# Performance work log

Measured on AMD Instinct MI355X. Metric: run time of the kernel, lower is better.

The kernel has to match this reference:

```python
import jax, jax.numpy as jnp
import numpy as np

TEMP = 1.0
EPS = 1e-15

B, N, F, K = 8, 2000, 128, 64


def setup_inputs() -> dict:
    key = jax.random.key(0)
    k1, k2, k3 = jax.random.split(key, 3)
    x = jax.random.normal(k1, (B, N, F), dtype=jnp.float32)
    adj = jax.random.uniform(k2, (B, N, N), dtype=jnp.float32)
    s = jax.random.normal(k3, (B, N, K), dtype=jnp.float32)
    mask = jnp.ones((B, N), dtype=bool)
    return {"x": x, "adj": adj, "s": s, "mask": mask}


def reference(x, adj, s, mask):
    k = s.shape[-1]
    s = jax.nn.softmax(s / TEMP, axis=-1)
    m = mask[..., None].astype(x.dtype)          # [B,N,1]
    x = x * m
    s = s * m

    # pooled features: s^T x -> [B,K,F]
    out = jnp.einsum('bnk,bnf->bkf', s, x)

    # pooled adjacency: s^T A s -> [B,K,K]
    as_ = jnp.einsum('bnm,bmk->bnk', adj, s)     # A s, [B,N,K]
    out_adj = jnp.einsum('bnk,bnl->bkl', as_, s)

    # mincut loss
    mincut_num = jnp.einsum('bkk->b', out_adj)
    d_flat = jnp.sum(adj, axis=-1)               # degree, [B,N]
    # trace(s^T diag(d) s) = sum_n d_n * sum_k s_nk^2 (avoids dense diag)
    mincut_den = jnp.einsum('bn,bnk,bnk->b', d_flat, s, s)
    mincut_loss = jnp.mean(-(mincut_num / mincut_den))

    # orthogonality loss
    ss = jnp.einsum('bnk,bnl->bkl', s, s)        # [B,K,K]
    ss_norm = jnp.linalg.norm(ss, axis=(-2, -1), keepdims=True)
    i_s = jnp.eye(k, dtype=ss.dtype)
    ortho = jnp.linalg.norm(ss / ss_norm - i_s / jnp.sqrt(jnp.asarray(k, ss.dtype)), axis=(-2, -1))
    ortho_loss = jnp.mean(ortho)

    # zero diagonal, symmetric degree normalization
    ind = jnp.arange(k)
    out_adj = out_adj.at[:, ind, ind].set(0.0)
    d = jnp.sqrt(jnp.sum(out_adj, axis=-1))[:, None, :] + EPS  # [B,1,K]
    out_adj = out_adj / d / jnp.swapaxes(d, 1, 2)

    return out, out_adj, mincut_loss, ortho_loss
```

## Files before the change

### kernel.cpp

```cpp
#include <hip/hip_runtime.h>

typedef __bf16 bf16;
typedef __bf16 bf16x4 __attribute__((ext_vector_type(4)));
typedef __bf16 bf16x8 __attribute__((ext_vector_type(8)));
typedef float f32x4 __attribute__((ext_vector_type(4)));

#define NB 8
#define NN 2000
#define N2 2048
#define KK 64
#define FF 128

__global__ __launch_bounds__(256) void k1_softmax(const float* __restrict__ s,
                                                  bf16* __restrict__ sT,
                                                  float* __restrict__ rowsq) {
  const int b = blockIdx.x >> 5, tile = blockIdx.x & 31;
  const int n0 = tile * 64;
  const int t = threadIdx.x;
  const int r = t >> 2, q = t & 3;
  __shared__ float ptile[64][65];
  const int n = n0 + r;
  const bool valid = n < NN;
  float v[16];
  if (valid) {
    const float4* src = (const float4*)(s + ((size_t)(b * NN + n)) * KK + q * 16);
#pragma unroll
    for (int i = 0; i < 4; ++i) {
      float4 f = src[i];
      v[4 * i + 0] = f.x; v[4 * i + 1] = f.y; v[4 * i + 2] = f.z; v[4 * i + 3] = f.w;
    }
  } else {
#pragma unroll
    for (int i = 0; i < 16; ++i) v[i] = 0.f;
  }
  float mx = v[0];
#pragma unroll
  for (int i = 1; i < 16; ++i) mx = fmaxf(mx, v[i]);
  mx = fmaxf(mx, __shfl_xor(mx, 1));
  mx = fmaxf(mx, __shfl_xor(mx, 2));
  float sum = 0.f;
#pragma unroll
  for (int i = 0; i < 16; ++i) { v[i] = __expf(v[i] - mx); sum += v[i]; }
  sum += __shfl_xor(sum, 1);
  sum += __shfl_xor(sum, 2);
  const float scale = valid ? (1.0f / sum) : 0.f;
  float rq = 0.f;
#pragma unroll
  for (int i = 0; i < 16; ++i) { v[i] *= scale; rq += v[i] * v[i]; }
  rq += __shfl_xor(rq, 1);
  rq += __shfl_xor(rq, 2);
  if (q == 0) rowsq[b * N2 + n0 + r] = rq;
#pragma unroll
  for (int i = 0; i < 16; ++i) ptile[r][q * 16 + i] = v[i];
  __syncthreads();
  bf16x8 o0, o1;
#pragma unroll
  for (int i = 0; i < 8; ++i) o0[i] = (bf16)ptile[q * 16 + i][r];
#pragma unroll
  for (int i = 0; i < 8; ++i) o1[i] = (bf16)ptile[q * 16 + 8 + i][r];
  bf16* dst = sT + ((size_t)(b * KK + r)) * N2 + n0 + q * 16;
  *(bf16x8*)dst = o0;
  *(bf16x8*)(dst + 8) = o1;
}

__global__ __launch_bounds__(1024, 8) void k2_big(const float* __restrict__ adj,
                                                  const bf16* __restrict__ sT,
                                                  const float* __restrict__ x,
                                                  bf16* __restrict__ xT,
                                                  bf16* __restrict__ asT,
                                                  const float* __restrict__ rowsq,
                                                  float* __restrict__ den_part) {
  __shared__ __align__(16) char smem[69632];
  __shared__ float dredS[16];
  const int bid0 = blockIdx.x;
  const int t = threadIdx.x;

  if (bid0 >= 256) {
    const int lg2 = ((bid0 - 256) & 7) * 32 + ((bid0 - 256) >> 3);
    const int bb = lg2 >> 5, tl = lg2 & 31;
    const int n0b = tl * 64;
    float* xt = (float*)smem;
#pragma unroll
    for (int i = 0; i < 2; ++i) {
      int idx = t + 1024 * i;
      int row = idx >> 5, c4 = idx & 31;
      int n = n0b + row;
      float4 vv = make_float4(0.f, 0.f, 0.f, 0.f);
      if (n < NN) vv = ((const float4*)(x + ((size_t)(bb * NN + n)) * FF))[c4];
      *(float4*)&xt[row * 132 + c4 * 4] = vv;
    }
    __syncthreads();
    const int f = t >> 3, h = t & 7;
    bf16x8 o;
#pragma unroll
    for (int i = 0; i < 8; ++i) o[i] = (bf16)xt[(h * 8 + i) * 132 + f];
    *(bf16x8*)(xT + ((size_t)(bb * FF + f)) * N2 + n0b + h * 8) = o;
    return;
  }

  const int lgc = (bid0 & 7) * 32 + (bid0 >> 3);
  const int b = lgc >> 5, tile = lgc & 31;
  const int n0 = tile * 64;

  const int w = t >> 6, l = t & 63;
  const int lr = l & 15, lg = l >> 4;
  const int nr = w & 3, kr = w >> 2;

  const int srow = t >> 4, scp = t & 15;
  const bool avalid = (n0 + srow) < NN;
  const float4* arowp = (const float4*)(adj +
      ((size_t)(b * NN) + (avalid ? (n0 + srow) : 0)) * NN);
  const bf16* sTrp = sT + ((size_t)(b * KK + srow)) * N2;

  const int afo = (nr * 16 + lr) * 136;
  const int bfo = 8704 + (kr * 16 + lr) * 136;

  f32x4 acc;
#pragma unroll
  for (int r = 0; r < 4; ++r) acc[r] = 0.f;

  float4 a0A, a1A, a0B, a1B;
  bf16x8 bA, bB;

#define K2_LOAD(C, LA0, LA1, LB)                                            \
  {                                                                         \
    const int base_ = (C) * 32 + scp * 2;                                   \
    const int i0_ = base_ > 499 ? 499 : base_;                              \
    const int i1_ = base_ + 1 > 499 ? 499 : base_ + 1;                      \
    if (avalid) { LA0 = arowp[i0_]; LA1 = arowp[i1_]; }                     \
    else { LA0 = make_float4(0.f,0.f,0.f,0.f); LA1 = LA0; }                 \
    LB = *(const bf16x8*)(sTrp + (C) * 128 + scp * 8);                      \
  }

#define K2_WRITE(BUF, LA0, LA1, LB)                                         \
  {                                                                         \
    bf16x8 av_;                                                             \
    av_[0] = (bf16)LA0.x; av_[1] = (bf16)LA0.y;                             \
    av_[2] = (bf16)LA0.z; av_[3] = (bf16)LA0.w;                             \
    av_[4] = (bf16)LA1.x; av_[5] = (bf16)LA1.y;                             \
    av_[6] = (bf16)LA1.z; av_[7] = (bf16)LA1.w;                             \
    bf16* p_ = (bf16*)smem + (BUF) * 17408 + srow * 136 + scp * 8;          \
    *(bf16x8*)p_ = av_;                                                     \
    *(bf16x8*)(p_ + 8704) = LB;                                             \
  }

#define K2_MFMA(BUF)                                                        \
  {                                                                         \
    const bf16* base_ = (bf16*)smem + (BUF) * 17408;                        \
    _Pragma("unroll")                                                       \
    for (int ms = 0; ms < 4; ++ms) {                                        \
      bf16x8 af_ = *(const bf16x8*)(base_ + afo + ms * 32 + lg * 8);        \
      bf16x8 bf_ = *(const bf16x8*)(base_ + bfo + ms * 32 + lg * 8);        \
      acc = __builtin_amdgcn_mfma_f32_16x16x32_bf16(af_, bf_, acc, 0, 0, 0);\
    }                                                                       \
  }

  K2_LOAD(0, a0A, a1A, bA);
  K2_WRITE(0, a0A, a1A, bA);
  K2_LOAD(1, a0B, a1B, bB);
  __syncthreads();
  for (int cc = 0; cc < 7; ++cc) {
    const int c = cc * 2;
    K2_LOAD(c + 2, a0A, a1A, bA);
    K2_MFMA(0);
    K2_WRITE(1, a0B, a1B, bB);
    __syncthreads();
    K2_LOAD(c + 3, a0B, a1B, bB);
    K2_MFMA(1);
    K2_WRITE(0, a0A, a1A, bA);
    __syncthreads();
  }
  K2_MFMA(0);
  K2_WRITE(1, a0B, a1B, bB);
  __syncthreads();
  K2_MFMA(1);
#undef K2_LOAD
#undef K2_WRITE
#undef K2_MFMA

  bf16x4 o;
#pragma unroll
  for (int r = 0; r < 4; ++r) o[r] = (bf16)acc[r];
  *(bf16x4*)(asT + ((size_t)(b * KK + kr * 16 + lr)) * N2 + n0 + nr * 16 + lg * 4) = o;

  float s0 = acc[0], s1 = acc[1], s2 = acc[2], s3 = acc[3];
#pragma unroll
  for (int off = 1; off <= 8; off <<= 1) {
    s0 += __shfl_xor(s0, off); s1 += __shfl_xor(s1, off);
    s2 += __shfl_xor(s2, off); s3 += __shfl_xor(s3, off);
  }
  const float* rqp = rowsq + b * N2 + n0 + nr * 16 + lg * 4;
  float part = s0 * rqp[0] + s1 * rqp[1] + s2 * rqp[2] + s3 * rqp[3];
  part += __shfl_xor(part, 16);
  part += __shfl_xor(part, 32);
  if (l == 0) dredS[w] = part;
  __syncthreads();
  if (t == 0) {
    float dt = 0.f;
#pragma unroll
    for (int i = 0; i < 16; ++i) dt += dredS[i];
    den_part[b * 32 + tile] = dt;
  }
}

__global__ __launch_bounds__(256) void k3_gemms(const bf16* __restrict__ sT,
                                                const bf16* __restrict__ asT,
                                                const bf16* __restrict__ xT,
                                                float* __restrict__ adjraw,
                                                float* __restrict__ ssw,
                                                float* __restrict__ dout) {
  const int lgc = (blockIdx.x & 7) * 64 + (blockIdx.x >> 3);
  const int b = lgc >> 6, u = lgc & 63;
  const bf16 *Ab, *Bb;
  float* Cb;
  int ldC;
  if (u < 16) {
    const int rt = u >> 2, ct = u & 3;
    Ab = asT + ((size_t)(b * KK + rt * 16)) * N2;
    Bb = sT + ((size_t)(b * KK + ct * 16)) * N2;
    Cb = adjraw + b * KK * KK + rt * 16 * KK + ct * 16; ldC = KK;
  } else if (u < 32) {
    const int v = u - 16, rt = v >> 2, ct = v & 3;
    Ab = sT + ((size_t)(b * KK + rt * 16)) * N2;
    Bb = sT + ((size_t)(b * KK + ct * 16)) * N2;
    Cb = ssw + b * KK * KK + rt * 16 * KK + ct * 16; ldC = KK;
  } else {
    const int v = u - 32, rt = v >> 3, ct = v & 7;
    Ab = sT + ((size_t)(b * KK + rt * 16)) * N2;
    Bb = xT + ((size_t)(b * FF + ct * 16)) * N2;
    Cb = dout + b * KK * FF + rt * 16 * FF + ct * 16; ldC = FF;
  }
  const int t = threadIdx.x;
  const int w = t >> 6, l = t & 63;
  const int lr = l & 15, lg = l >> 4;
  f32x4 acc;
#pragma unroll
  for (int r = 0; r < 4; ++r) acc[r] = 0.f;
  const int m_begin = w * 512;
#pragma unroll 4
  for (int s = 0; s < 16; ++s) {
    const int m = m_begin + s * 32 + lg * 8;
    bf16x8 af = *(const bf16x8*)(Ab + (size_t)lr * N2 + m);
    bf16x8 bfv = *(const bf16x8*)(Bb + (size_t)lr * N2 + m);
    acc = __builtin_amdgcn_mfma_f32_16x16x32_bf16(af, bfv, acc, 0, 0, 0);
  }
  __shared__ float red[4][16][16];
#pragma unroll
  for (int r = 0; r < 4; ++r) red[w][lg * 4 + r][lr] = acc[r];
  __syncthreads();
  const int row = t >> 4, col = t & 15;
  const float v = red[0][row][col] + red[1][row][col] +
                  red[2][row][col] + red[3][row][col];
  Cb[row * ldC + col] = v;
}

__device__ inline float wred64(float v) {
#pragma unroll
  for (int off = 32; off > 0; off >>= 1) v += __shfl_xor(v, off);
  return v;
}

__global__ __launch_bounds__(512) void k4_final(const float* __restrict__ adjraw,
                                                const float* __restrict__ ssw,
                                                const float* __restrict__ den_part,
                                                float* __restrict__ dout) {
  const int b = threadIdx.x >> 6;
  const int lane = threadIdx.x & 63;
  const float dp = (lane < 32) ? den_part[b * 32 + lane] : 0.f;
  const float den = wred64(dp);
  const float* arow = adjraw + b * 4096 + lane * 64;
  float4 av[16];
#pragma unroll
  for (int i = 0; i < 16; ++i) av[i] = ((const float4*)arow)[i];
  const float diag = adjraw[b * 4096 + lane * 65];
  float rs = 0.f;
#pragma unroll
  for (int i = 0; i < 16; ++i) rs += av[i].x + av[i].y + av[i].z + av[i].w;
  rs -= diag;
  rs = fmaxf(rs, 0.f);
  const float num = wred64(diag);
  const float d = sqrtf(rs) + 1e-15f;
  __shared__ float dsh[8][64];
  __shared__ float lossm[8], losso[8];
  dsh[b][lane] = d;
  __syncthreads();
  const float invd = 1.0f / d;
  float* orow = dout + NB * KK * FF + b * 4096 + lane * 64;
#pragma unroll
  for (int i = 0; i < 16; ++i) {
    float4 cvv = av[i];
    cvv.x = (4 * i + 0 == lane) ? 0.f : cvv.x * invd / dsh[b][4 * i + 0];
    cvv.y = (4 * i + 1 == lane) ? 0.f : cvv.y * invd / dsh[b][4 * i + 1];
    cvv.z = (4 * i + 2 == lane) ? 0.f : cvv.z * invd / dsh[b][4 * i + 2];
    cvv.w = (4 * i + 3 == lane) ? 0.f : cvv.w * invd / dsh[b][4 * i + 3];
    ((float4*)orow)[i] = cvv;
  }
  const float* srow = ssw + b * 4096 + lane * 64;
  float4 sv[16];
  float sq = 0.f;
#pragma unroll
  for (int i = 0; i < 16; ++i) {
    sv[i] = ((const float4*)srow)[i];
    sq += sv[i].x * sv[i].x + sv[i].y * sv[i].y + sv[i].z * sv[i].z + sv[i].w * sv[i].w;
  }
  const float frob = sqrtf(wred64(sq));
  const float fi = 1.0f / frob;
  float osum = 0.f;
#pragma unroll
  for (int i = 0; i < 16; ++i) {
    float tx = sv[i].x * fi - ((4 * i + 0 == lane) ? 0.125f : 0.f);
    float ty = sv[i].y * fi - ((4 * i + 1 == lane) ? 0.125f : 0.f);
    float tz = sv[i].z * fi - ((4 * i + 2 == lane) ? 0.125f : 0.f);
    float tw = sv[i].w * fi - ((4 * i + 3 == lane) ? 0.125f : 0.f);
    osum += tx * tx + ty * ty + tz * tz + tw * tw;
  }
  const float ot = wred64(osum);
  if (lane == 0) {
    lossm[b] = -(num / den);
    losso[b] = sqrtf(ot);
  }
  __syncthreads();
  if (threadIdx.x == 0) {
    float m = 0.f, oo = 0.f;
#pragma unroll
    for (int b2 = 0; b2 < 8; ++b2) { m += lossm[b2]; oo += losso[b2]; }
    dout[NB * KK * FF + NB * KK * KK + 0] = m * 0.125f;
    dout[NB * KK * FF + NB * KK * KK + 1] = oo * 0.125f;
  }
}

extern "C" void kernel_launch(void* const* d_in, const int* in_sizes, int n_in,
                              void* d_out, int out_size, void* d_ws, size_t ws_size,
                              hipStream_t stream) {
  const float* x = (const float*)d_in[0];
  const float* adj = (const float*)d_in[1];
  const float* s = (const float*)d_in[2];
  float* out = (float*)d_out;
  char* ws = (char*)d_ws;
  bf16* sT = (bf16*)ws;
  bf16* xT = (bf16*)(ws + (2u << 20));
  bf16* asT = (bf16*)(ws + (6u << 20));
  float* rowsq = (float*)(ws + (8u << 20));
  float* den_part = (float*)(ws + (8u << 20) + 65536);
  float* adjraw = (float*)(ws + (8u << 20) + 65536 + 4096);
  float* ssw = adjraw + NB * KK * KK;

  k1_softmax<<<256, 256, 0, stream>>>(s, sT, rowsq);
  k2_big<<<512, 1024, 0, stream>>>(adj, sT, x, xT, asT, rowsq, den_part);
  k3_gemms<<<512, 256, 0, stream>>>(sT, asT, xT, adjraw, ssw, out);
  k4_final<<<1, 512, 0, stream>>>(adjraw, ssw, den_part, out);
}
```

Measured before the change: 228.4 us.

## Split A·s GEMM into 32-row tiles with 512-thread blocks for more parallelism

The adjacency-times-assignment GEMM kernel now processes 32 rows of adj per block instead of 64, using 512 threads and 512 GEMM blocks (plus 256 x-transpose blocks) instead of 256+256. The sT operand tile is loaded redundantly per block, and the denominator partial sums go to 64 slots per batch instead of 32. The double-buffered pipeline becomes a single loop with fewer unrolled stages. The aim is to spread the memory-bound adj stream over more CUs and improve occupancy, at the cost of re-reading s twice as often and a smaller per-block reuse.

```diff
diff --git a/kernel.cpp b/kernel.cpp
--- a/kernel.cpp
+++ b/kernel.cpp
@@ -63,26 +63,26 @@
   *(bf16x8*)(dst + 8) = o1;
 }
 
-__global__ __launch_bounds__(1024, 8) void k2_big(const float* __restrict__ adj,
-                                                  const bf16* __restrict__ sT,
-                                                  const float* __restrict__ x,
-                                                  bf16* __restrict__ xT,
-                                                  bf16* __restrict__ asT,
-                                                  const float* __restrict__ rowsq,
-                                                  float* __restrict__ den_part) {
-  __shared__ __align__(16) char smem[69632];
-  __shared__ float dredS[16];
+__global__ __launch_bounds__(512, 6) void k2_big(const float* __restrict__ adj,
+                                                 const bf16* __restrict__ sT,
+                                                 const float* __restrict__ x,
+                                                 bf16* __restrict__ xT,
+                                                 bf16* __restrict__ asT,
+                                                 const float* __restrict__ rowsq,
+                                                 float* __restrict__ den_part) {
+  __shared__ __align__(16) char smem[52224];
+  __shared__ float dredS[8];
   const int bid0 = blockIdx.x;
   const int t = threadIdx.x;
 
-  if (bid0 >= 256) {
-    const int lg2 = ((bid0 - 256) & 7) * 32 + ((bid0 - 256) >> 3);
-    const int bb = lg2 >> 5, tl = lg2 & 31;
+  if (bid0 >= 512) {
+    const int q = bid0 - 512;
+    const int bb = q & 7, tl = q >> 3;
     const int n0b = tl * 64;
     float* xt = (float*)smem;
 #pragma unroll
-    for (int i = 0; i < 2; ++i) {
-      int idx = t + 1024 * i;
+    for (int i = 0; i < 4; ++i) {
+      int idx = t + 512 * i;
       int row = idx >> 5, c4 = idx & 31;
       int n = n0b + row;
       float4 vv = make_float4(0.f, 0.f, 0.f, 0.f);
@@ -90,63 +90,69 @@
       *(float4*)&xt[row * 132 + c4 * 4] = vv;
     }
     __syncthreads();
-    const int f = t >> 3, h = t & 7;
-    bf16x8 o;
-#pragma unroll
-    for (int i = 0; i < 8; ++i) o[i] = (bf16)xt[(h * 8 + i) * 132 + f];
-    *(bf16x8*)(xT + ((size_t)(bb * FF + f)) * N2 + n0b + h * 8) = o;
+    const int f = t >> 2, h = t & 3;
+    bf16x8 o0, o1;
+#pragma unroll
+    for (int i = 0; i < 8; ++i) o0[i] = (bf16)xt[(h * 16 + i) * 132 + f];
+#pragma unroll
+    for (int i = 0; i < 8; ++i) o1[i] = (bf16)xt[(h * 16 + 8 + i) * 132 + f];
+    bf16* dst = xT + ((size_t)(bb * FF + f)) * N2 + n0b + h * 16;
+    *(bf16x8*)dst = o0;
+    *(bf16x8*)(dst + 8) = o1;
     return;
   }
 
-  const int lgc = (bid0 & 7) * 32 + (bid0 >> 3);
-  const int b = lgc >> 5, tile = lgc & 31;
-  const int n0 = tile * 64;
+  const int b = bid0 & 7, tile = bid0 >> 3;
+  const int n0 = tile * 32;
 
   const int w = t >> 6, l = t & 63;
   const int lr = l & 15, lg = l >> 4;
-  const int nr = w & 3, kr = w >> 2;
+  const int nr = w & 1, kr = w >> 1;
 
   const int srow = t >> 4, scp = t & 15;
+  const int brow = t >> 3, bcol = t & 7;
   const bool avalid = (n0 + srow) < NN;
   const float4* arowp = (const float4*)(adj +
       ((size_t)(b * NN) + (avalid ? (n0 + srow) : 0)) * NN);
-  const bf16* sTrp = sT + ((size_t)(b * KK + srow)) * N2;
+  const bf16* sTrp = sT + ((size_t)(b * KK + brow)) * N2;
 
   const int afo = (nr * 16 + lr) * 136;
-  const int bfo = 8704 + (kr * 16 + lr) * 136;
+  const int bfo = 4352 + (kr * 16 + lr) * 136;
 
   f32x4 acc;
 #pragma unroll
   for (int r = 0; r < 4; ++r) acc[r] = 0.f;
 
-  float4 a0A, a1A, a0B, a1B;
-  bf16x8 bA, bB;
-
-#define K2_LOAD(C, LA0, LA1, LB)                                            \
+  float4 La0, La1;
+  bf16x8 Lb0, Lb1;
+
+#define K2_LOAD(C)                                                          \
   {                                                                         \
     const int base_ = (C) * 32 + scp * 2;                                   \
     const int i0_ = base_ > 499 ? 499 : base_;                              \
     const int i1_ = base_ + 1 > 499 ? 499 : base_ + 1;                      \
-    if (avalid) { LA0 = arowp[i0_]; LA1 = arowp[i1_]; }                     \
-    else { LA0 = make_float4(0.f,0.f,0.f,0.f); LA1 = LA0; }                 \
-    LB = *(const bf16x8*)(sTrp + (C) * 128 + scp * 8);                      \
-  }
-
-#define K2_WRITE(BUF, LA0, LA1, LB)                                         \
-  {                                                                         \
-    bf16x8 av_;                                                             \
-    av_[0] = (bf16)LA0.x; av_[1] = (bf16)LA0.y;                             \
-    av_[2] = (bf16)LA0.z; av_[3] = (bf16)LA0.w;                             \
-    av_[4] = (bf16)LA1.x; av_[5] = (bf16)LA1.y;                             \
-    av_[6] = (bf16)LA1.z; av_[7] = (bf16)LA1.w;                             \
-    bf16* p_ = (bf16*)smem + (BUF) * 17408 + srow * 136 + scp * 8;          \
-    *(bf16x8*)p_ = av_;                                                     \
-    *(bf16x8*)(p_ + 8704) = LB;                                             \
+    if (avalid) { La0 = arowp[i0_]; La1 = arowp[i1_]; }                     \
+    else { La0 = make_float4(0.f,0.f,0.f,0.f); La1 = La0; }                 \
+    Lb0 = *(const bf16x8*)(sTrp + (C) * 128 + bcol * 8);                    \
+    Lb1 = *(const bf16x8*)(sTrp + (C) * 128 + 64 + bcol * 8);               \
+  }
+
+#define K2_WRITE(BUF)                                                      \
+  {                                                                        \
+    bf16x8 av_;                                                            \
+    av_[0] = (bf16)La0.x; av_[1] = (bf16)La0.y;                            \
+    av_[2] = (bf16)La0.z; av_[3] = (bf16)La0.w;                            \
+    av_[4] = (bf16)La1.x; av_[5] = (bf16)La1.y;                            \
+    av_[6] = (bf16)La1.z; av_[7] = (bf16)La1.w;                            \
+    bf16* bb_ = (bf16*)smem + (BUF) * 13056;                               \
+    *(bf16x8*)(bb_ + srow * 136 + scp * 8) = av_;                          \
+    *(bf16x8*)(bb_ + 4352 + brow * 136 + bcol * 8) = Lb0;                  \
+    *(bf16x8*)(bb_ + 4352 + brow * 136 + 64 + bcol * 8) = Lb1;             \
   }
 
 #define K2_MFMA(BUF)                                                        \
   {                                                                         \
-    const bf16* base_ = (bf16*)smem + (BUF) * 17408;                        \
+    const bf16* base_ = (bf16*)smem + (BUF) * 13056;                        \
     _Pragma("unroll")                                                       \
     for (int ms = 0; ms < 4; ++ms) {                                        \
       bf16x8 af_ = *(const bf16x8*)(base_ + afo + ms * 32 + lg * 8);        \
@@ -155,25 +161,15 @@
     }                                                                       \
   }
 
-  K2_LOAD(0, a0A, a1A, bA);
-  K2_WRITE(0, a0A, a1A, bA);
-  K2_LOAD(1, a0B, a1B, bB);
-  __syncthreads();
-  for (int cc = 0; cc < 7; ++cc) {
-    const int c = cc * 2;
-    K2_LOAD(c + 2, a0A, a1A, bA);
-    K2_MFMA(0);
-    K2_WRITE(1, a0B, a1B, bB);
+  K2_LOAD(0);
+  K2_WRITE(0);
+  __syncthreads();
+  for (int c = 0; c < 16; ++c) {
+    if (c < 15) K2_LOAD(c + 1);
+    K2_MFMA(c & 1);
+    if (c < 15) K2_WRITE((c + 1) & 1);
     __syncthreads();
-    K2_LOAD(c + 3, a0B, a1B, bB);
-    K2_MFMA(1);
-    K2_WRITE(0, a0A, a1A, bA);
-    __syncthreads();
-  }
-  K2_MFMA(0);
-  K2_WRITE(1, a0B, a1B, bB);
-  __syncthreads();
-  K2_MFMA(1);
+  }
 #undef K2_LOAD
 #undef K2_WRITE
 #undef K2_MFMA
@@ -198,8 +194,8 @@
   if (t == 0) {
     float dt = 0.f;
 #pragma unroll
-    for (int i = 0; i < 16; ++i) dt += dredS[i];
-    den_part[b * 32 + tile] = dt;
+    for (int i = 0; i < 8; ++i) dt += dredS[i];
+    den_part[b * 64 + tile] = dt;
   }
 }
 
@@ -266,8 +262,7 @@
                                                 float* __restrict__ dout) {
   const int b = threadIdx.x >> 6;
   const int lane = threadIdx.x & 63;
-  const float dp = (lane < 32) ? den_part[b * 32 + lane] : 0.f;
-  const float den = wred64(dp);
+  const float den = wred64(den_part[b * 64 + lane]);
   const float* arow = adjraw + b * 4096 + lane * 64;
   float4 av[16];
 #pragma unroll
@@ -346,7 +341,7 @@
   float* ssw = adjraw + NB * KK * KK;
 
   k1_softmax<<<256, 256, 0, stream>>>(s, sT, rowsq);
-  k2_big<<<512, 1024, 0, stream>>>(adj, sT, x, xT, asT, rowsq, den_part);
+  k2_big<<<768, 512, 0, stream>>>(adj, sT, x, xT, asT, rowsq, den_part);
   k3_gemms<<<512, 256, 0, stream>>>(sT, asT, xT, adjraw, ssw, out);
   k4_final<<<1, 512, 0, stream>>>(adjraw, ssw, den_part, out);
 }
```

After: 230.5 us. Within noise of the previous version (+0.9%).

## Split adjacency GEMM along reduction dim into two halves for more blocks

Applied to the files above, without the earlier changes.

The A·s GEMM in k2 is split along the m (reduction) dimension into two halves, doubling the number of GEMM blocks from 256 to 512 so more CUs are busy streaming adj. Each half writes fp32 partial results to a new asP buffer, and k3 sums the two partials before converting to bf16 for the s^T(As) product. Degree-denominator partials are also split, and k4 reduces 64 entries instead of 32. This trades extra fp32 partial writes and reads, plus a larger workspace, for better occupancy on the memory-bound adj stream.

```diff
diff --git a/kernel.cpp b/kernel.cpp
--- a/kernel.cpp
+++ b/kernel.cpp
@@ -67,7 +67,7 @@
                                                   const bf16* __restrict__ sT,
                                                   const float* __restrict__ x,
                                                   bf16* __restrict__ xT,
-                                                  bf16* __restrict__ asT,
+                                                  float* __restrict__ asP,
                                                   const float* __restrict__ rowsq,
                                                   float* __restrict__ den_part) {
   __shared__ __align__(16) char smem[69632];
@@ -75,8 +75,9 @@
   const int bid0 = blockIdx.x;
   const int t = threadIdx.x;
 
-  if (bid0 >= 256) {
-    const int lg2 = ((bid0 - 256) & 7) * 32 + ((bid0 - 256) >> 3);
+  if (bid0 >= 512) {
+    const int q = bid0 - 512;
+    const int lg2 = (q & 7) * 32 + (q >> 3);
     const int bb = lg2 >> 5, tl = lg2 & 31;
     const int n0b = tl * 64;
     float* xt = (float*)smem;
@@ -98,9 +99,12 @@
     return;
   }
 
-  const int lgc = (bid0 & 7) * 32 + (bid0 >> 3);
-  const int b = lgc >> 5, tile = lgc & 31;
+  const int b = bid0 & 7;
+  const int idx = bid0 >> 3;
+  const int tile = idx & 31, half = idx >> 5;
   const int n0 = tile * 64;
+  const int mb4 = half * 256;
+  const int mbE = half * 1024;
 
   const int w = t >> 6, l = t & 63;
   const int lr = l & 15, lg = l >> 4;
@@ -119,29 +123,29 @@
 #pragma unroll
   for (int r = 0; r < 4; ++r) acc[r] = 0.f;
 
-  float4 a0A, a1A, a0B, a1B;
-  bf16x8 bA, bB;
-
-#define K2_LOAD(C, LA0, LA1, LB)                                            \
+  float4 La0, La1;
+  bf16x8 Lb;
+
+#define K2_LOAD(C)                                                          \
   {                                                                         \
-    const int base_ = (C) * 32 + scp * 2;                                   \
+    const int base_ = mb4 + (C) * 32 + scp * 2;                             \
     const int i0_ = base_ > 499 ? 499 : base_;                              \
     const int i1_ = base_ + 1 > 499 ? 499 : base_ + 1;                      \
-    if (avalid) { LA0 = arowp[i0_]; LA1 = arowp[i1_]; }                     \
-    else { LA0 = make_float4(0.f,0.f,0.f,0.f); LA1 = LA0; }                 \
-    LB = *(const bf16x8*)(sTrp + (C) * 128 + scp * 8);                      \
-  }
-
-#define K2_WRITE(BUF, LA0, LA1, LB)                                         \
+    if (avalid) { La0 = arowp[i0_]; La1 = arowp[i1_]; }                     \
+    else { La0 = make_float4(0.f,0.f,0.f,0.f); La1 = La0; }                 \
+    Lb = *(const bf16x8*)(sTrp + mbE + (C) * 128 + scp * 8);                \
+  }
+
+#define K2_WRITE(BUF)                                                       \
   {                                                                         \
     bf16x8 av_;                                                             \
-    av_[0] = (bf16)LA0.x; av_[1] = (bf16)LA0.y;                             \
-    av_[2] = (bf16)LA0.z; av_[3] = (bf16)LA0.w;                             \
-    av_[4] = (bf16)LA1.x; av_[5] = (bf16)LA1.y;                             \
-    av_[6] = (bf16)LA1.z; av_[7] = (bf16)LA1.w;                             \
+    av_[0] = (bf16)La0.x; av_[1] = (bf16)La0.y;                             \
+    av_[2] = (bf16)La0.z; av_[3] = (bf16)La0.w;                             \
+    av_[4] = (bf16)La1.x; av_[5] = (bf16)La1.y;                             \
+    av_[6] = (bf16)La1.z; av_[7] = (bf16)La1.w;                             \
     bf16* p_ = (bf16*)smem + (BUF) * 17408 + srow * 136 + scp * 8;          \
     *(bf16x8*)p_ = av_;                                                     \
-    *(bf16x8*)(p_ + 8704) = LB;                                             \
+    *(bf16x8*)(p_ + 8704) = Lb;                                             \
   }
 
 #define K2_MFMA(BUF)                                                        \
@@ -155,33 +159,21 @@
     }                                                                       \
   }
 
-  K2_LOAD(0, a0A, a1A, bA);
-  K2_WRITE(0, a0A, a1A, bA);
-  K2_LOAD(1, a0B, a1B, bB);
-  __syncthreads();
-  for (int cc = 0; cc < 7; ++cc) {
-    const int c = cc * 2;
-    K2_LOAD(c + 2, a0A, a1A, bA);
-    K2_MFMA(0);
-    K2_WRITE(1, a0B, a1B, bB);
+  K2_LOAD(0);
+  K2_WRITE(0);
+  __syncthreads();
+  for (int c = 0; c < 8; ++c) {
+    if (c < 7) K2_LOAD(c + 1);
+    K2_MFMA(c & 1);
+    if (c < 7) K2_WRITE((c + 1) & 1);
     __syncthreads();
-    K2_LOAD(c + 3, a0B, a1B, bB);
-    K2_MFMA(1);
-    K2_WRITE(0, a0A, a1A, bA);
-    __syncthreads();
-  }
-  K2_MFMA(0);
-  K2_WRITE(1, a0B, a1B, bB);
-  __syncthreads();
-  K2_MFMA(1);
+  }
 #undef K2_LOAD
 #undef K2_WRITE
 #undef K2_MFMA
 
-  bf16x4 o;
-#pragma unroll
-  for (int r = 0; r < 4; ++r) o[r] = (bf16)acc[r];
-  *(bf16x4*)(asT + ((size_t)(b * KK + kr * 16 + lr)) * N2 + n0 + nr * 16 + lg * 4) = o;
+  *(f32x4*)(asP + ((size_t)((half * NB + b) * KK + kr * 16 + lr)) * N2 +
+            n0 + nr * 16 + lg * 4) = acc;
 
   float s0 = acc[0], s1 = acc[1], s2 = acc[2], s3 = acc[3];
 #pragma unroll
@@ -199,50 +191,68 @@
     float dt = 0.f;
 #pragma unroll
     for (int i = 0; i < 16; ++i) dt += dredS[i];
-    den_part[b * 32 + tile] = dt;
+    den_part[b * 64 + half * 32 + tile] = dt;
   }
 }
 
 __global__ __launch_bounds__(256) void k3_gemms(const bf16* __restrict__ sT,
-                                                const bf16* __restrict__ asT,
+                                                const float* __restrict__ asP,
                                                 const bf16* __restrict__ xT,
                                                 float* __restrict__ adjraw,
                                                 float* __restrict__ ssw,
                                                 float* __restrict__ dout) {
   const int lgc = (blockIdx.x & 7) * 64 + (blockIdx.x >> 3);
   const int b = lgc >> 6, u = lgc & 63;
-  const bf16 *Ab, *Bb;
+  const int t = threadIdx.x;
+  const int w = t >> 6, l = t & 63;
+  const int lr = l & 15, lg = l >> 4;
+  const int m_begin = w * 512;
+  f32x4 acc;
+#pragma unroll
+  for (int r = 0; r < 4; ++r) acc[r] = 0.f;
   float* Cb;
   int ldC;
   if (u < 16) {
     const int rt = u >> 2, ct = u & 3;
-    Ab = asT + ((size_t)(b * KK + rt * 16)) * N2;
-    Bb = sT + ((size_t)(b * KK + ct * 16)) * N2;
+    const float* A0 = asP + ((size_t)(b * KK + rt * 16)) * N2 + (size_t)lr * N2;
+    const float* A1 = asP + ((size_t)((NB + b) * KK + rt * 16)) * N2 + (size_t)lr * N2;
+    const bf16* Bb = sT + ((size_t)(b * KK + ct * 16)) * N2 + (size_t)lr * N2;
     Cb = adjraw + b * KK * KK + rt * 16 * KK + ct * 16; ldC = KK;
-  } else if (u < 32) {
-    const int v = u - 16, rt = v >> 2, ct = v & 3;
-    Ab = sT + ((size_t)(b * KK + rt * 16)) * N2;
-    Bb = sT + ((size_t)(b * KK + ct * 16)) * N2;
-    Cb = ssw + b * KK * KK + rt * 16 * KK + ct * 16; ldC = KK;
+#pragma unroll 4
+    for (int s = 0; s < 16; ++s) {
+      const int m = m_begin + s * 32 + lg * 8;
+      f32x4 x0 = *(const f32x4*)(A0 + m);
+      f32x4 x1 = *(const f32x4*)(A0 + m + 4);
+      f32x4 y0 = *(const f32x4*)(A1 + m);
+      f32x4 y1 = *(const f32x4*)(A1 + m + 4);
+      bf16x8 af;
+      af[0] = (bf16)(x0[0] + y0[0]); af[1] = (bf16)(x0[1] + y0[1]);
+      af[2] = (bf16)(x0[2] + y0[2]); af[3] = (bf16)(x0[3] + y0[3]);
+      af[4] = (bf16)(x1[0] + y1[0]); af[5] = (bf16)(x1[1] + y1[1]);
+      af[6] = (bf16)(x1[2] + y1[2]); af[7] = (bf16)(x1[3] + y1[3]);
+      bf16x8 bfv = *(const bf16x8*)(Bb + m);
+      acc = __builtin_amdgcn_mfma_f32_16x16x32_bf16(af, bfv, acc, 0, 0, 0);
+    }
   } else {
-    const int v = u - 32, rt = v >> 3, ct = v & 7;
-    Ab = sT + ((size_t)(b * KK + rt * 16)) * N2;
-    Bb = xT + ((size_t)(b * FF + ct * 16)) * N2;
-    Cb = dout + b * KK * FF + rt * 16 * FF + ct * 16; ldC = FF;
-  }
-  const int t = threadIdx.x;
-  const int w = t >> 6, l = t & 63;
-  const int lr = l & 15, lg = l >> 4;
-  f32x4 acc;
-#pragma unroll
-  for (int r = 0; r < 4; ++r) acc[r] = 0.f;
-  const int m_begin = w * 512;
+    const bf16 *Ab, *Bb;
+    if (u < 32) {
+      const int v = u - 16, rt = v >> 2, ct = v & 3;
+      Ab = sT + ((size_t)(b * KK + rt * 16)) * N2;
+      Bb = sT + ((size_t)(b * KK + ct * 16)) * N2;
+      Cb = ssw + b * KK * KK + rt * 16 * KK + ct * 16; ldC = KK;
+    } else {
+      const int v = u - 32, rt = v >> 3, ct = v & 7;
+      Ab = sT + ((size_t)(b * KK + rt * 16)) * N2;
+      Bb = xT + ((size_t)(b * FF + ct * 16)) * N2;
+      Cb = dout + b * KK * FF + rt * 16 * FF + ct * 16; ldC = FF;
+    }
 #pragma unroll 4
-  for (int s = 0; s < 16; ++s) {
-    const int m = m_begin + s * 32 + lg * 8;
-    bf16x8 af = *(const bf16x8*)(Ab + (size_t)lr * N2 + m);
-    bf16x8 bfv = *(const bf16x8*)(Bb + (size_t)lr * N2 + m);
-    acc = __builtin_amdgcn_mfma_f32_16x16x32_bf16(af, bfv, acc, 0, 0, 0);
+    for (int s = 0; s < 16; ++s) {
+      const int m = m_begin + s * 32 + lg * 8;
+      bf16x8 af = *(const bf16x8*)(Ab + (size_t)lr * N2 + m);
+      bf16x8 bfv = *(const bf16x8*)(Bb + (size_t)lr * N2 + m);
+      acc = __builtin_amdgcn_mfma_f32_16x16x32_bf16(af, bfv, acc, 0, 0, 0);
+    }
   }
   __shared__ float red[4][16][16];
 #pragma unroll
@@ -266,8 +276,7 @@
                                                 float* __restrict__ dout) {
   const int b = threadIdx.x >> 6;
   const int lane = threadIdx.x & 63;
-  const float dp = (lane < 32) ? den_part[b * 32 + lane] : 0.f;
-  const float den = wred64(dp);
+  const float den = wred64(den_part[b * 64 + lane]);
   const float* arow = adjraw + b * 4096 + lane * 64;
   float4 av[16];
 #pragma unroll
@@ -339,14 +348,14 @@
   char* ws = (char*)d_ws;
   bf16* sT = (bf16*)ws;
   bf16* xT = (bf16*)(ws + (2u << 20));
-  bf16* asT = (bf16*)(ws + (6u << 20));
-  float* rowsq = (float*)(ws + (8u << 20));
-  float* den_part = (float*)(ws + (8u << 20) + 65536);
-  float* adjraw = (float*)(ws + (8u << 20) + 65536 + 4096);
+  float* asP = (float*)(ws + (6u << 20));
+  float* rowsq = (float*)(ws + (14u << 20));
+  float* den_part = (float*)(ws + (14u << 20) + 65536);
+  float* adjraw = (float*)(ws + (14u << 20) + 65536 + 4096);
   float* ssw = adjraw + NB * KK * KK;
 
   k1_softmax<<<256, 256, 0, stream>>>(s, sT, rowsq);
-  k2_big<<<512, 1024, 0, stream>>>(adj, sT, x, xT, asT, rowsq, den_part);
-  k3_gemms<<<512, 256, 0, stream>>>(sT, asT, xT, adjraw, ssw, out);
+  k2_big<<<768, 1024, 0, stream>>>(adj, sT, x, xT, asP, rowsq, den_part);
+  k3_gemms<<<512, 256, 0, stream>>>(sT, asP, xT, adjraw, ssw, out);
   k4_final<<<1, 512, 0, stream>>>(adjraw, ssw, den_part, out);
 }
```

Result: slower. 233.6 us (+2.3%).
